# Performance work log

Measured on AMD Instinct MI355X. Metric: run time of the kernel, lower is better.

## Reference

```python
import jax, jax.numpy as jnp
import numpy as np


def setup_inputs() -> dict:
    key = jax.random.key(0)
    ks = jax.random.split(key, 20)
    B, P, ENC = 128, 196, 512
    DEC, ATT, EMB, V, S1 = 512, 256, 256, 5000, 257
    s = 0.02
    inp = {
        "features": jax.random.normal(ks[0], (B, P, ENC), jnp.float32),
        "captions": jax.random.randint(ks[1], (B, S1), 0, V),
        "emb": jax.random.normal(ks[2], (V, EMB), jnp.float32) * s,
        "Ua_w": jax.random.normal(ks[3], (ENC, ATT), jnp.float32) * s,
        "Ua_b": jnp.zeros((ATT,), jnp.float32),
        "Wa_w": jax.random.normal(ks[4], (DEC, ATT), jnp.float32) * s,
        "Wa_b": jnp.zeros((ATT,), jnp.float32),
        "va_w": jax.random.normal(ks[5], (ATT,), jnp.float32) * s,
        "va_b": jnp.zeros((), jnp.float32),
        "ih_w": jax.random.normal(ks[6], (ENC, DEC), jnp.float32) * s,
        "ih_b": jnp.zeros((DEC,), jnp.float32),
        "ic_w": jax.random.normal(ks[7], (ENC, DEC), jnp.float32) * s,
        "ic_b": jnp.zeros((DEC,), jnp.float32),
        "W_ih": jax.random.normal(ks[8], (EMB + ENC, 4 * DEC), jnp.float32) * s,
        "b_ih": jnp.zeros((4 * DEC,), jnp.float32),
        "W_hh": jax.random.normal(ks[9], (DEC, 4 * DEC), jnp.float32) * s,
        "b_hh": jnp.zeros((4 * DEC,), jnp.float32),
        "fcn_w": jax.random.normal(ks[10], (DEC, V), jnp.float32) * s,
        "fcn_b": jnp.zeros((V,), jnp.float32),
    }
    return inp


def reference(features, captions, emb, Ua_w, Ua_b, Wa_w, Wa_b, va_w, va_b,
              ih_w, ih_b, ic_w, ic_b, W_ih, b_ih, W_hh, b_hh, fcn_w, fcn_b):
    # embeds: [B, S+1, E]; we consume embeds[:, :S]
    embeds = emb[captions]
    mean_f = features.mean(axis=1)                      # [B, ENC]
    h0 = mean_f @ ih_w + ih_b                           # [B, DEC]
    c0 = mean_f @ ic_w + ic_b
    Uf = features @ Ua_w + Ua_b                         # [B, P, ATT] precomputed

    def step(carry, x_emb):
        h, c = carry
        att = jnp.tanh(Uf + (h @ Wa_w + Wa_b)[:, None, :])   # [B, P, ATT]
        scores = att @ va_w + va_b                            # [B, P]
        alpha = jax.nn.softmax(scores, axis=1)
        context = jnp.einsum('bp,bpe->be', alpha, features)   # [B, ENC]
        x = jnp.concatenate([x_emb, context], axis=1)         # [B, EMB+ENC]
        gates = x @ W_ih + b_ih + h @ W_hh + b_hh             # [B, 4*DEC]
        i, f, g, o = jnp.split(gates, 4, axis=1)
        c = jax.nn.sigmoid(f) * c + jax.nn.sigmoid(i) * jnp.tanh(g)
        h = jax.nn.sigmoid(o) * jnp.tanh(c)
        out = h @ fcn_w + fcn_b                               # dropout is identity (p=0)
        return (h, c), out

    xs = jnp.swapaxes(embeds[:, :-1], 0, 1)             # [S, B, EMB]
    _, preds = jax.lax.scan(step, (h0, c0), xs)         # [S, B, V]
    return jnp.swapaxes(preds, 0, 1)                    # [B, S, V]
```

## Files before the change

kernel.cpp:

```cpp
#include <hip/hip_runtime.h>
#include <hip/hip_bf16.h>

#define B 128
#define P 196
#define PP 200
#define ENC 512
#define DEC 512
#define ATT 256
#define EMB 256
#define V 5000
#define S 256
#define S1 257
#define NG 2048
#define KS 16

typedef __attribute__((ext_vector_type(4))) short s4v;
typedef __attribute__((ext_vector_type(8))) short s8v;

__device__ __forceinline__ float bf2f(short u) {
    unsigned int x = ((unsigned int)(unsigned short)u) << 16;
    float f; __builtin_memcpy(&f, &x, 4); return f;
}

__global__ __launch_bounds__(256) void k_mean(const float* __restrict__ feat,
                                              float* __restrict__ mean_f) {
    int idx = blockIdx.x * 256 + threadIdx.x;
    int b = idx >> 9, e = idx & 511;
    const float* fp = feat + (size_t)b * P * ENC + e;
    float s = 0.f;
    for (int p = 0; p < P; ++p) s += fp[(size_t)p * ENC];
    mean_f[idx] = s * (1.0f / (float)P);
}

__global__ __launch_bounds__(256) void k_init_hc(const float* __restrict__ mean_f,
        const float* __restrict__ ih_w, const float* __restrict__ ih_b,
        const float* __restrict__ ic_w, const float* __restrict__ ic_b,
        float* __restrict__ h, float* __restrict__ c) {
    int idx = blockIdx.x * 256 + threadIdx.x;
    int b = idx >> 9, d = idx & 511;
    const float* mf = mean_f + (size_t)b * ENC;
    float sh = ih_b[d], sc = ic_b[d];
    for (int e = 0; e < ENC; ++e) {
        float m = mf[e];
        sh = fmaf(m, ih_w[(size_t)e * DEC + d], sh);
        sc = fmaf(m, ic_w[(size_t)e * DEC + d], sc);
    }
    h[idx] = sh; c[idx] = sc;
}

__global__ __launch_bounds__(256) void k_uf(const float* __restrict__ feat,
        const float* __restrict__ Ua_w, const float* __restrict__ Ua_b,
        __hip_bfloat16* __restrict__ Uf) {
    int row0 = blockIdx.x * 8;
    int a = threadIdx.x;
    __shared__ float fs[8][ENC];
    for (int i = threadIdx.x; i < 8 * ENC; i += 256) {
        int r = i >> 9, e = i & 511;
        fs[r][e] = feat[(size_t)(row0 + r) * ENC + e];
    }
    __syncthreads();
    float acc[8];
    float bia = Ua_b[a];
#pragma unroll
    for (int r = 0; r < 8; ++r) acc[r] = bia;
    for (int e = 0; e < ENC; ++e) {
        float w = Ua_w[(size_t)e * ATT + a];
#pragma unroll
        for (int r = 0; r < 8; ++r) acc[r] = fmaf(fs[r][e], w, acc[r]);
    }
#pragma unroll
    for (int r = 0; r < 8; ++r)
        Uf[(size_t)(row0 + r) * ATT + a] = __float2bfloat16(acc[r]);
}

__global__ __launch_bounds__(512) void k_featT(const float* __restrict__ feat,
        __hip_bfloat16* __restrict__ featT) {
    int b = blockIdx.x, p0 = blockIdx.y * 8;
    int e = threadIdx.x;
    __hip_bfloat16 v[8];
#pragma unroll
    for (int i = 0; i < 8; ++i) {
        int p = p0 + i;
        float f = (p < P) ? feat[((size_t)b * P + p) * ENC + e] : 0.f;
        v[i] = __float2bfloat16(f);
    }
    __builtin_memcpy(&featT[((size_t)b * ENC + e) * PP + p0], v, 16);
}

__global__ __launch_bounds__(256) void k_wacvt(const float* __restrict__ w,
        __hip_bfloat16* __restrict__ wb) {
    int i = blockIdx.x * 256 + threadIdx.x;
    wb[i] = __float2bfloat16(w[i]);
}

__global__ __launch_bounds__(256) void k_gemb(const float* __restrict__ emb,
        const int* __restrict__ captions, const float* __restrict__ W_ih,
        __hip_bfloat16* __restrict__ Gemb) {
    __shared__ float As[16][128];
    __shared__ float Bs[16][128];
    __shared__ int rowcap[128];
    int m0 = blockIdx.x * 128;
    int n0 = blockIdx.y * 128;
    int tid = threadIdx.x;
    if (tid < 128) {
        int m = m0 + tid;
        rowcap[tid] = captions[(size_t)(m & 127) * S1 + (m >> 7)];
    }
    __syncthreads();
    int tx = tid & 15, ty = tid >> 4;
    float acc[8][8];
#pragma unroll
    for (int i = 0; i < 8; ++i)
#pragma unroll
        for (int j = 0; j < 8; ++j) acc[i][j] = 0.f;
    int arow = tid >> 1, ak = (tid & 1) * 8;
    int bkk = tid >> 4, bn = (tid & 15) * 8;
    for (int k0 = 0; k0 < EMB; k0 += 16) {
        {
            const float* ap = emb + (size_t)rowcap[arow] * EMB + k0 + ak;
            float4 v0 = *(const float4*)ap;
            float4 v1 = *(const float4*)(ap + 4);
            As[ak + 0][arow] = v0.x; As[ak + 1][arow] = v0.y;
            As[ak + 2][arow] = v0.z; As[ak + 3][arow] = v0.w;
            As[ak + 4][arow] = v1.x; As[ak + 5][arow] = v1.y;
            As[ak + 6][arow] = v1.z; As[ak + 7][arow] = v1.w;
        }
        {
            const float* bp = W_ih + (size_t)(k0 + bkk) * NG + n0 + bn;
            *(float4*)&Bs[bkk][bn] = *(const float4*)bp;
            *(float4*)&Bs[bkk][bn + 4] = *(const float4*)(bp + 4);
        }
        __syncthreads();
#pragma unroll
        for (int kk = 0; kk < 16; ++kk) {
            float4 a0 = *(const float4*)&As[kk][ty * 8];
            float4 a1 = *(const float4*)&As[kk][ty * 8 + 4];
            float4 b0 = *(const float4*)&Bs[kk][tx * 8];
            float4 b1 = *(const float4*)&Bs[kk][tx * 8 + 4];
            float av[8] = {a0.x, a0.y, a0.z, a0.w, a1.x, a1.y, a1.z, a1.w};
            float bv[8] = {b0.x, b0.y, b0.z, b0.w, b1.x, b1.y, b1.z, b1.w};
#pragma unroll
            for (int i = 0; i < 8; ++i)
#pragma unroll
                for (int j = 0; j < 8; ++j)
                    acc[i][j] = fmaf(av[i], bv[j], acc[i][j]);
        }
        __syncthreads();
    }
#pragma unroll
    for (int i = 0; i < 8; ++i) {
        __hip_bfloat16* gp = Gemb + (size_t)(m0 + ty * 8 + i) * NG + n0 + tx * 8;
#pragma unroll
        for (int j = 0; j < 8; ++j) gp[j] = __float2bfloat16(acc[i][j]);
    }
}

__global__ __launch_bounds__(1024) void k_attn_cell(
        const float* __restrict__ partials, const __hip_bfloat16* __restrict__ Gemb,
        const float* __restrict__ b_ih, const float* __restrict__ b_hh,
        float* __restrict__ h, const float* __restrict__ cr, float* __restrict__ cw,
        float* __restrict__ Hall,
        const __hip_bfloat16* __restrict__ Wa_wb, const float* __restrict__ Wa_b,
        const __hip_bfloat16* __restrict__ Uf, const __hip_bfloat16* __restrict__ featT,
        const float* __restrict__ va_w, const float* __restrict__ va_b,
        float* __restrict__ ctxp, float* __restrict__ mlp,
        int t, int use_gemb, int use_hall) {
    int g = blockIdx.x;
    int b = g >> 1, half = g & 1;
    int tid = threadIdx.x;
    int base = half ? 96 : 0;
    int cnt  = half ? 100 : 96;
    __shared__ float hs[DEC];
    __shared__ float wahp[4][ATT];
    __shared__ float wahs[ATT];
    __shared__ float sc[104];
    __shared__ float red[4];
    __shared__ float cpart[2][ENC];

    if (t > 0) {
        if (tid < DEC) {
            int d = tid;
            float s0 = b_ih[d]           + b_hh[d];
            float s1 = b_ih[d + DEC]     + b_hh[d + DEC];
            float s2 = b_ih[d + 2 * DEC] + b_hh[d + 2 * DEC];
            float s3 = b_ih[d + 3 * DEC] + b_hh[d + 3 * DEC];
#pragma unroll
            for (int ks = 0; ks < KS; ++ks) {
                const float* pp = partials + ((size_t)ks * B + b) * NG + d;
                s0 += pp[0]; s1 += pp[DEC]; s2 += pp[2 * DEC]; s3 += pp[3 * DEC];
            }
            if (use_gemb) {
                const __hip_bfloat16* gp = Gemb + ((size_t)(t - 1) * B + b) * NG + d;
                s0 += __bfloat162float(gp[0]);
                s1 += __bfloat162float(gp[DEC]);
                s2 += __bfloat162float(gp[2 * DEC]);
                s3 += __bfloat162float(gp[3 * DEC]);
            }
            size_t gidx = (size_t)b * DEC + d;
            float ii = 1.f / (1.f + __expf(-s0));
            float ff = 1.f / (1.f + __expf(-s1));
            float gg = tanhf(s2);
            float oo = 1.f / (1.f + __expf(-s3));
            float cn = ff * cr[gidx] + ii * gg;
            float hn = oo * tanhf(cn);
            hs[d] = hn;
            if (half == 0) {
                cw[gidx] = cn;
                h[gidx] = hn;
                if (use_hall) Hall[((size_t)(t - 1) * B + b) * DEC + d] = hn;
            }
        }
    } else {
        if (tid < DEC) hs[tid] = h[(size_t)b * DEC + tid];
    }
    __syncthreads();
    if (t == S) return;

    {
        int a = tid & 255, q = tid >> 8;
        float acc = 0.f;
        const __hip_bfloat16* wp = Wa_wb + (size_t)(q * 128) * ATT + a;
        const float* hq = &hs[q * 128];
#pragma unroll 4
        for (int dd = 0; dd < 128; ++dd)
            acc = fmaf(hq[dd], bf2f(*(const short*)&wp[(size_t)dd * ATT]), acc);
        wahp[q][a] = acc;
    }
    __syncthreads();
    if (tid < ATT)
        wahs[tid] = Wa_b[tid] + wahp[0][tid] + wahp[1][tid] + wahp[2][tid] + wahp[3][tid];
    __syncthreads();

    {
        int w = tid >> 6, lane = tid & 63;
        float4 wv = *(const float4*)&wahs[lane * 4];
        float4 vv = *(const float4*)&va_w[lane * 4];
        float vb = va_b[0];
        for (int pl = w; pl < cnt; pl += 16) {
            const __hip_bfloat16* ufp = Uf + ((size_t)b * P + base + pl) * ATT + lane * 4;
            s4v u4 = *(const s4v*)ufp;
            float ssc = vv.x * tanhf(bf2f(u4.x) + wv.x) + vv.y * tanhf(bf2f(u4.y) + wv.y)
                      + vv.z * tanhf(bf2f(u4.z) + wv.z) + vv.w * tanhf(bf2f(u4.w) + wv.w);
#pragma unroll
            for (int off = 32; off; off >>= 1) ssc += __shfl_down(ssc, off);
            if (lane == 0) sc[pl] = ssc + vb;
        }
    }
    __syncthreads();

    {
        int lane = tid & 63;
        float v = (tid < cnt) ? sc[tid] : -1e30f;
        if (tid < 128) {
            float m = v;
#pragma unroll
            for (int off = 32; off; off >>= 1) m = fmaxf(m, __shfl_down(m, off));
            if (lane == 0) red[tid >> 6] = m;
        }
        __syncthreads();
        float mh = fmaxf(red[0], red[1]);
        float e = (tid < cnt) ? __expf(v - mh) : 0.f;
        if (tid < 128) {
            float l = e;
#pragma unroll
            for (int off = 32; off; off >>= 1) l += __shfl_down(l, off);
            if (lane == 0) red[2 + (tid >> 6)] = l;
        }
        __syncthreads();
        if (tid < cnt) sc[tid] = e;
        else if (tid < 104) sc[tid] = 0.f;
        if (tid == 0) {
            mlp[((size_t)half * B + b) * 2 + 0] = mh;
            mlp[((size_t)half * B + b) * 2 + 1] = red[2] + red[3];
        }
    }
    __syncthreads();

    {
        int e = tid & 511, ph = tid >> 9;
        int start = half ? (ph ? 7 : 0) : (ph ? 6 : 0);
        int nch   = half ? (ph ? 6 : 7) : 6;
        float acc = 0.f;
        const __hip_bfloat16* fr = featT + ((size_t)b * ENC + e) * PP + base + start * 8;
        for (int ch = 0; ch < nch; ++ch) {
            s8v raw = *(const s8v*)(fr + ch * 8);
            const float* sp = &sc[(start + ch) * 8];
#pragma unroll
            for (int j = 0; j < 8; ++j)
                acc = fmaf(sp[j], bf2f(raw[j]), acc);
        }
        cpart[ph][e] = acc;
    }
    __syncthreads();
    if (tid < ENC)
        ctxp[((size_t)half * B + b) * ENC + tid] = cpart[0][tid] + cpart[1][tid];
}

__global__ __launch_bounds__(256) void k_gates(const float* __restrict__ emb,
        const int* __restrict__ captions, int t,
        const float* __restrict__ ctxp, const float* __restrict__ mlp,
        const float* __restrict__ h,
        const float* __restrict__ W_ih, const float* __restrict__ W_hh,
        float* __restrict__ partials, int use_gemb) {
    __shared__ float As[16][128];
    __shared__ float Bs[16][64];
    __shared__ float sw0[B], sw1[B];
    __shared__ int scap[B];
    int n0 = blockIdx.x * 64;
    int ks = blockIdx.y;
    int tid = threadIdx.x;
    int kch = use_gemb ? 64 : 80;
    if (tid < B) {
        float m0 = mlp[(size_t)tid * 2 + 0];
        float l0 = mlp[(size_t)tid * 2 + 1];
        float m1 = mlp[((size_t)B + tid) * 2 + 0];
        float l1 = mlp[((size_t)B + tid) * 2 + 1];
        float M = fmaxf(m0, m1);
        float e0 = __expf(m0 - M), e1 = __expf(m1 - M);
        float inv = 1.f / (l0 * e0 + l1 * e1);
        sw0[tid] = e0 * inv; sw1[tid] = e1 * inv;
        if (!use_gemb) scap[tid] = captions[(size_t)tid * S1 + t];
    }
    __syncthreads();
    int tx = tid & 15, ty = tid >> 4;
    float acc[8][4];
#pragma unroll
    for (int i = 0; i < 8; ++i)
#pragma unroll
        for (int j = 0; j < 4; ++j) acc[i][j] = 0.f;
    int arow = tid >> 1, ak = (tid & 1) * 8;
    int bkk = tid >> 4, bn = (tid & 15) * 4;
    for (int k0 = ks * kch; k0 < ks * kch + kch; k0 += 16) {
        {
            int k = k0 + ak;
            if (!use_gemb && k < EMB) {
                const float* ap = emb + (size_t)scap[arow] * EMB + k;
                float4 v0 = *(const float4*)ap;
                float4 v1 = *(const float4*)(ap + 4);
                As[ak + 0][arow] = v0.x; As[ak + 1][arow] = v0.y;
                As[ak + 2][arow] = v0.z; As[ak + 3][arow] = v0.w;
                As[ak + 4][arow] = v1.x; As[ak + 5][arow] = v1.y;
                As[ak + 6][arow] = v1.z; As[ak + 7][arow] = v1.w;
            } else {
                int kc = use_gemb ? k : (k - EMB);
                if (kc < ENC) {
                    const float* p0 = ctxp + (size_t)arow * ENC + kc;
                    const float* p1 = ctxp + ((size_t)B + arow) * ENC + kc;
                    float w0 = sw0[arow], w1 = sw1[arow];
                    float4 a0 = *(const float4*)p0;
                    float4 a1 = *(const float4*)(p0 + 4);
                    float4 b0 = *(const float4*)p1;
                    float4 b1 = *(const float4*)(p1 + 4);
                    As[ak + 0][arow] = a0.x * w0 + b0.x * w1;
                    As[ak + 1][arow] = a0.y * w0 + b0.y * w1;
                    As[ak + 2][arow] = a0.z * w0 + b0.z * w1;
                    As[ak + 3][arow] = a0.w * w0 + b0.w * w1;
                    As[ak + 4][arow] = a1.x * w0 + b1.x * w1;
                    As[ak + 5][arow] = a1.y * w0 + b1.y * w1;
                    As[ak + 6][arow] = a1.z * w0 + b1.z * w1;
                    As[ak + 7][arow] = a1.w * w0 + b1.w * w1;
                } else {
                    const float* ap = h + (size_t)arow * DEC + (kc - ENC);
                    float4 v0 = *(const float4*)ap;
                    float4 v1 = *(const float4*)(ap + 4);
                    As[ak + 0][arow] = v0.x; As[ak + 1][arow] = v0.y;
                    As[ak + 2][arow] = v0.z; As[ak + 3][arow] = v0.w;
                    As[ak + 4][arow] = v1.x; As[ak + 5][arow] = v1.y;
                    As[ak + 6][arow] = v1.z; As[ak + 7][arow] = v1.w;
                }
            }
        }
        {
            int k = k0 + bkk;
            const float* bp;
            if (use_gemb)
                bp = (k < ENC) ? W_ih + (size_t)(k + EMB) * NG + n0 + bn
                               : W_hh + (size_t)(k - ENC) * NG + n0 + bn;
            else
                bp = (k < EMB + ENC) ? W_ih + (size_t)k * NG + n0 + bn
                                     : W_hh + (size_t)(k - EMB - ENC) * NG + n0 + bn;
            *(float4*)&Bs[bkk][bn] = *(const float4*)bp;
        }
        __syncthreads();
#pragma unroll
        for (int kk = 0; kk < 16; ++kk) {
            float4 a0 = *(const float4*)&As[kk][ty * 8];
            float4 a1 = *(const float4*)&As[kk][ty * 8 + 4];
            float4 b0 = *(const float4*)&Bs[kk][tx * 4];
            float av[8] = {a0.x, a0.y, a0.z, a0.w, a1.x, a1.y, a1.z, a1.w};
            float bv[4] = {b0.x, b0.y, b0.z, b0.w};
#pragma unroll
            for (int i = 0; i < 8; ++i)
#pragma unroll
                for (int j = 0; j < 4; ++j)
                    acc[i][j] = fmaf(av[i], bv[j], acc[i][j]);
        }
        __syncthreads();
    }
#pragma unroll
    for (int i = 0; i < 8; ++i) {
        int mrow = ty * 8 + i;
        float* pp = partials + ((size_t)ks * B + mrow) * NG + n0 + tx * 4;
        *(float4*)pp = make_float4(acc[i][0], acc[i][1], acc[i][2], acc[i][3]);
    }
}

__global__ __launch_bounds__(256) void k_fcn(const float* __restrict__ A,
        const float* __restrict__ Bw, const float* __restrict__ bias,
        float* __restrict__ out, int t_fix) {
    __shared__ float As[16][128];
    __shared__ float Bs[16][128];
    int m0 = blockIdx.x * 128;
    int n0 = blockIdx.y * 128;
    int tid = threadIdx.x;
    int tx = tid & 15, ty = tid >> 4;
    float acc[8][8];
#pragma unroll
    for (int i = 0; i < 8; ++i)
#pragma unroll
        for (int j = 0; j < 8; ++j) acc[i][j] = 0.f;
    int arow = tid >> 1, ak = (tid & 1) * 8;
    int bkk = tid >> 4, bn = (tid & 15) * 8;
    const float4 z4 = make_float4(0.f, 0.f, 0.f, 0.f);
    for (int k0 = 0; k0 < DEC; k0 += 16) {
        {
            const float* ap = A + (size_t)(m0 + arow) * DEC + k0 + ak;
            float4 v0 = *(const float4*)ap;
            float4 v1 = *(const float4*)(ap + 4);
            As[ak + 0][arow] = v0.x; As[ak + 1][arow] = v0.y;
            As[ak + 2][arow] = v0.z; As[ak + 3][arow] = v0.w;
            As[ak + 4][arow] = v1.x; As[ak + 5][arow] = v1.y;
            As[ak + 6][arow] = v1.z; As[ak + 7][arow] = v1.w;
        }
        {
            int n4 = n0 + bn;
            const float* bp = Bw + (size_t)(k0 + bkk) * V + n4;
            float4 v0 = (n4 < V) ? *(const float4*)bp : z4;
            float4 v1 = (n4 + 4 < V) ? *(const float4*)(bp + 4) : z4;
            *(float4*)&Bs[bkk][bn] = v0;
            *(float4*)&Bs[bkk][bn + 4] = v1;
        }
        __syncthreads();
#pragma unroll
        for (int kk = 0; kk < 16; ++kk) {
            float4 a0 = *(const float4*)&As[kk][ty * 8];
            float4 a1 = *(const float4*)&As[kk][ty * 8 + 4];
            float4 b0 = *(const float4*)&Bs[kk][tx * 8];
            float4 b1 = *(const float4*)&Bs[kk][tx * 8 + 4];
            float av[8] = {a0.x, a0.y, a0.z, a0.w, a1.x, a1.y, a1.z, a1.w};
            float bv[8] = {b0.x, b0.y, b0.z, b0.w, b1.x, b1.y, b1.z, b1.w};
#pragma unroll
            for (int i = 0; i < 8; ++i)
#pragma unroll
                for (int j = 0; j < 8; ++j)
                    acc[i][j] = fmaf(av[i], bv[j], acc[i][j]);
        }
        __syncthreads();
    }
#pragma unroll
    for (int i = 0; i < 8; ++i) {
        int mrow = m0 + ty * 8 + i;
        int bb, tt;
        if (t_fix >= 0) { bb = mrow; tt = t_fix; }
        else            { tt = mrow >> 7; bb = mrow & 127; }
        float* op = out + ((size_t)bb * S + tt) * V + n0 + tx * 8;
#pragma unroll
        for (int j = 0; j < 8; ++j) {
            int n = n0 + tx * 8 + j;
            if (n < V) op[j] = acc[i][j] + bias[n];
        }
    }
}

extern "C" void kernel_launch(void* const* d_in, const int* in_sizes, int n_in,
                              void* d_out, int out_size, void* d_ws, size_t ws_size,
                              hipStream_t stream) {
    const float* features = (const float*)d_in[0];
    const int*   captions = (const int*)d_in[1];
    const float* emb      = (const float*)d_in[2];
    const float* Ua_w     = (const float*)d_in[3];
    const float* Ua_b     = (const float*)d_in[4];
    const float* Wa_w     = (const float*)d_in[5];
    const float* Wa_b     = (const float*)d_in[6];
    const float* va_w     = (const float*)d_in[7];
    const float* va_b     = (const float*)d_in[8];
    const float* ih_w     = (const float*)d_in[9];
    const float* ih_b     = (const float*)d_in[10];
    const float* ic_w     = (const float*)d_in[11];
    const float* ic_b     = (const float*)d_in[12];
    const float* W_ih     = (const float*)d_in[13];
    const float* b_ih     = (const float*)d_in[14];
    const float* W_hh     = (const float*)d_in[15];
    const float* b_hh     = (const float*)d_in[16];
    const float* fcn_w    = (const float*)d_in[17];
    const float* fcn_b    = (const float*)d_in[18];
    float* out = (float*)d_out;
    char* wsb  = (char*)d_ws;

    size_t off = 0;
    __hip_bfloat16* Uf    = (__hip_bfloat16*)(wsb + off); off += (size_t)B * P * ATT * 2;
    __hip_bfloat16* featT = (__hip_bfloat16*)(wsb + off); off += (size_t)B * ENC * PP * 2;
    __hip_bfloat16* Wa_wb = (__hip_bfloat16*)(wsb + off); off += (size_t)DEC * ATT * 2;
    float* partials = (float*)(wsb + off); off += (size_t)KS * B * NG * 4;
    float* hbuf     = (float*)(wsb + off); off += (size_t)B * DEC * 4;
    float* cbufA    = (float*)(wsb + off); off += (size_t)B * DEC * 4;
    float* cbufB    = (float*)(wsb + off); off += (size_t)B * DEC * 4;
    float* ctxp     = (float*)(wsb + off); off += (size_t)2 * B * ENC * 4;
    float* mlp      = (float*)(wsb + off); off += 4096;
    float* meanf    = ctxp;
    size_t need_min = off;
    float* Hall     = (float*)(wsb + off); off += (size_t)S * B * DEC * 4;
    size_t need_hall = off;
    __hip_bfloat16* Gemb = (__hip_bfloat16*)(wsb + off);
    off += (size_t)S * B * NG * 2;
    size_t need_gemb = off;

    (void)need_min;
    int use_hall = ws_size >= need_hall;
    int use_gemb = ws_size >= need_gemb;

    k_mean<<<256, 256, 0, stream>>>(features, meanf);
    k_init_hc<<<256, 256, 0, stream>>>(meanf, ih_w, ih_b, ic_w, ic_b, hbuf, cbufA);
    k_uf<<<3136, 256, 0, stream>>>(features, Ua_w, Ua_b, Uf);
    k_featT<<<dim3(128, 25), 512, 0, stream>>>(features, featT);
    k_wacvt<<<512, 256, 0, stream>>>(Wa_w, Wa_wb);
    if (use_gemb)
        k_gemb<<<dim3(256, 16), 256, 0, stream>>>(emb, captions, W_ih, Gemb);

    for (int t = 0; t <= S; ++t) {
        const float* crd = (t & 1) ? cbufA : cbufB;
        float*       cwr = (t & 1) ? cbufB : cbufA;
        k_attn_cell<<<256, 1024, 0, stream>>>(partials, Gemb, b_ih, b_hh,
                hbuf, crd, cwr, Hall, Wa_wb, Wa_b, Uf, featT, va_w, va_b,
                ctxp, mlp, t, use_gemb, use_hall);
        if (t < S)
            k_gates<<<dim3(32, KS), 256, 0, stream>>>(emb, captions, t, ctxp, mlp,
                    hbuf, W_ih, W_hh, partials, use_gemb);
        if (!use_hall && t > 0)
            k_fcn<<<dim3(1, 40), 256, 0, stream>>>(hbuf, fcn_w, fcn_b, out, t - 1);
    }
    if (use_hall)
        k_fcn<<<dim3(256, 40), 256, 0, stream>>>(Hall, fcn_w, fcn_b, out, -1);
}
```

Before: 14.77 ms.

## Double-buffer gates GEMM, prefetch Uf into LDS, use fast tanh

The gates GEMM kernel now keeps two shared-memory buffers and loads the next K-chunk into registers while computing on the current one, leaving one barrier per chunk instead of two. In the attention-cell kernel, threads 512-1023 copy the per-batch Uf slice into LDS while the first 512 threads finish the LSTM cell update, and the score loop then reads Uf from LDS. tanhf is replaced with a clamped exp/rcp approximation in the cell and attention paths. This adds LDS usage (about 51KB for ufs) and slightly changes numerics.

```diff
diff --git a/kernel.cpp b/kernel.cpp
--- a/kernel.cpp
+++ b/kernel.cpp
@@ -20,6 +20,12 @@
 __device__ __forceinline__ float bf2f(short u) {
     unsigned int x = ((unsigned int)(unsigned short)u) << 16;
     float f; __builtin_memcpy(&f, &x, 4); return f;
+}
+
+__device__ __forceinline__ float tanhf_fast(float x) {
+    float xx = fminf(fmaxf(x, -15.f), 15.f);
+    float t = __expf(2.f * xx);
+    return (t - 1.f) * __builtin_amdgcn_rcpf(t + 1.f);
 }
 
 __global__ __launch_bounds__(256) void k_mean(const float* __restrict__ feat,
@@ -170,6 +176,7 @@
     int tid = threadIdx.x;
     int base = half ? 96 : 0;
     int cnt  = half ? 100 : 96;
+    __shared__ short ufs[100][ATT];
     __shared__ float hs[DEC];
     __shared__ float wahp[4][ATT];
     __shared__ float wahs[ATT];
@@ -177,8 +184,8 @@
     __shared__ float red[4];
     __shared__ float cpart[2][ENC];
 
-    if (t > 0) {
-        if (tid < DEC) {
+    if (tid < 512) {
+        if (t > 0) {
             int d = tid;
             float s0 = b_ih[d]           + b_hh[d];
             float s1 = b_ih[d + DEC]     + b_hh[d + DEC];
@@ -199,19 +206,25 @@
             size_t gidx = (size_t)b * DEC + d;
             float ii = 1.f / (1.f + __expf(-s0));
             float ff = 1.f / (1.f + __expf(-s1));
-            float gg = tanhf(s2);
+            float gg = tanhf_fast(s2);
             float oo = 1.f / (1.f + __expf(-s3));
             float cn = ff * cr[gidx] + ii * gg;
-            float hn = oo * tanhf(cn);
+            float hn = oo * tanhf_fast(cn);
             hs[d] = hn;
             if (half == 0) {
                 cw[gidx] = cn;
                 h[gidx] = hn;
                 if (use_hall) Hall[((size_t)(t - 1) * B + b) * DEC + d] = hn;
             }
-        }
-    } else {
-        if (tid < DEC) hs[tid] = h[(size_t)b * DEC + tid];
+        } else {
+            hs[tid] = h[(size_t)b * DEC + tid];
+        }
+    } else if (t < S) {
+        const __hip_bfloat16* ub = Uf + ((size_t)b * P + base) * ATT;
+        for (int i = tid - 512; i < cnt * 32; i += 512) {
+            int p = i >> 5, c = (i & 31) * 8;
+            *(s8v*)&ufs[p][c] = *(const s8v*)(ub + (size_t)p * ATT + c);
+        }
     }
     __syncthreads();
     if (t == S) return;
@@ -237,10 +250,11 @@
         float4 vv = *(const float4*)&va_w[lane * 4];
         float vb = va_b[0];
         for (int pl = w; pl < cnt; pl += 16) {
-            const __hip_bfloat16* ufp = Uf + ((size_t)b * P + base + pl) * ATT + lane * 4;
-            s4v u4 = *(const s4v*)ufp;
-            float ssc = vv.x * tanhf(bf2f(u4.x) + wv.x) + vv.y * tanhf(bf2f(u4.y) + wv.y)
-                      + vv.z * tanhf(bf2f(u4.z) + wv.z) + vv.w * tanhf(bf2f(u4.w) + wv.w);
+            s4v u4 = *(const s4v*)&ufs[pl][lane * 4];
+            float ssc = vv.x * tanhf_fast(bf2f(u4.x) + wv.x)
+                      + vv.y * tanhf_fast(bf2f(u4.y) + wv.y)
+                      + vv.z * tanhf_fast(bf2f(u4.z) + wv.z)
+                      + vv.w * tanhf_fast(bf2f(u4.w) + wv.w);
 #pragma unroll
             for (int off = 32; off; off >>= 1) ssc += __shfl_down(ssc, off);
             if (lane == 0) sc[pl] = ssc + vb;
@@ -302,8 +316,8 @@
         const float* __restrict__ h,
         const float* __restrict__ W_ih, const float* __restrict__ W_hh,
         float* __restrict__ partials, int use_gemb) {
-    __shared__ float As[16][128];
-    __shared__ float Bs[16][64];
+    __shared__ float As[2][16][128];
+    __shared__ float Bs[2][16][64];
     __shared__ float sw0[B], sw1[B];
     __shared__ int scap[B];
     int n0 = blockIdx.x * 64;
@@ -321,7 +335,6 @@
         sw0[tid] = e0 * inv; sw1[tid] = e1 * inv;
         if (!use_gemb) scap[tid] = captions[(size_t)tid * S1 + t];
     }
-    __syncthreads();
     int tx = tid & 15, ty = tid >> 4;
     float acc[8][4];
 #pragma unroll
@@ -330,17 +343,69 @@
         for (int j = 0; j < 4; ++j) acc[i][j] = 0.f;
     int arow = tid >> 1, ak = (tid & 1) * 8;
     int bkk = tid >> 4, bn = (tid & 15) * 4;
-    for (int k0 = ks * kch; k0 < ks * kch + kch; k0 += 16) {
-        {
+    int kbase = ks * kch;
+    int nch = kch >> 4;
+    float rA[8];
+    float4 rB;
+    __syncthreads();
+
+    {
+        int k = kbase + ak;
+        if (!use_gemb && k < EMB) {
+            const float* ap = emb + (size_t)scap[arow] * EMB + k;
+            float4 v0 = *(const float4*)ap;
+            float4 v1 = *(const float4*)(ap + 4);
+            rA[0] = v0.x; rA[1] = v0.y; rA[2] = v0.z; rA[3] = v0.w;
+            rA[4] = v1.x; rA[5] = v1.y; rA[6] = v1.z; rA[7] = v1.w;
+        } else {
+            int kc = use_gemb ? k : (k - EMB);
+            if (kc < ENC) {
+                const float* p0 = ctxp + (size_t)arow * ENC + kc;
+                const float* p1 = ctxp + ((size_t)B + arow) * ENC + kc;
+                float w0 = sw0[arow], w1 = sw1[arow];
+                float4 a0 = *(const float4*)p0;
+                float4 a1 = *(const float4*)(p0 + 4);
+                float4 b0 = *(const float4*)p1;
+                float4 b1 = *(const float4*)(p1 + 4);
+                rA[0] = a0.x * w0 + b0.x * w1; rA[1] = a0.y * w0 + b0.y * w1;
+                rA[2] = a0.z * w0 + b0.z * w1; rA[3] = a0.w * w0 + b0.w * w1;
+                rA[4] = a1.x * w0 + b1.x * w1; rA[5] = a1.y * w0 + b1.y * w1;
+                rA[6] = a1.z * w0 + b1.z * w1; rA[7] = a1.w * w0 + b1.w * w1;
+            } else {
+                const float* ap = h + (size_t)arow * DEC + (kc - ENC);
+                float4 v0 = *(const float4*)ap;
+                float4 v1 = *(const float4*)(ap + 4);
+                rA[0] = v0.x; rA[1] = v0.y; rA[2] = v0.z; rA[3] = v0.w;
+                rA[4] = v1.x; rA[5] = v1.y; rA[6] = v1.z; rA[7] = v1.w;
+            }
+        }
+        int kb = kbase + bkk;
+        const float* bp;
+        if (use_gemb)
+            bp = (kb < ENC) ? W_ih + (size_t)(kb + EMB) * NG + n0 + bn
+                            : W_hh + (size_t)(kb - ENC) * NG + n0 + bn;
+        else
+            bp = (kb < EMB + ENC) ? W_ih + (size_t)kb * NG + n0 + bn
+                                  : W_hh + (size_t)(kb - EMB - ENC) * NG + n0 + bn;
+        rB = *(const float4*)bp;
+    }
+#pragma unroll
+    for (int i = 0; i < 8; ++i) As[0][ak + i][arow] = rA[i];
+    *(float4*)&Bs[0][bkk][bn] = rB;
+    __syncthreads();
+
+    for (int c = 0; c < nch; ++c) {
+        int cur = c & 1;
+        bool more = (c + 1 < nch);
+        if (more) {
+            int k0 = kbase + (c + 1) * 16;
             int k = k0 + ak;
             if (!use_gemb && k < EMB) {
                 const float* ap = emb + (size_t)scap[arow] * EMB + k;
                 float4 v0 = *(const float4*)ap;
                 float4 v1 = *(const float4*)(ap + 4);
-                As[ak + 0][arow] = v0.x; As[ak + 1][arow] = v0.y;
-                As[ak + 2][arow] = v0.z; As[ak + 3][arow] = v0.w;
-                As[ak + 4][arow] = v1.x; As[ak + 5][arow] = v1.y;
-                As[ak + 6][arow] = v1.z; As[ak + 7][arow] = v1.w;
+                rA[0] = v0.x; rA[1] = v0.y; rA[2] = v0.z; rA[3] = v0.w;
+                rA[4] = v1.x; rA[5] = v1.y; rA[6] = v1.z; rA[7] = v1.w;
             } else {
                 int kc = use_gemb ? k : (k - EMB);
                 if (kc < ENC) {
@@ -351,42 +416,33 @@
                     float4 a1 = *(const float4*)(p0 + 4);
                     float4 b0 = *(const float4*)p1;
                     float4 b1 = *(const float4*)(p1 + 4);
-                    As[ak + 0][arow] = a0.x * w0 + b0.x * w1;
-                    As[ak + 1][arow] = a0.y * w0 + b0.y * w1;
-                    As[ak + 2][arow] = a0.z * w0 + b0.z * w1;
-                    As[ak + 3][arow] = a0.w * w0 + b0.w * w1;
-                    As[ak + 4][arow] = a1.x * w0 + b1.x * w1;
-                    As[ak + 5][arow] = a1.y * w0 + b1.y * w1;
-                    As[ak + 6][arow] = a1.z * w0 + b1.z * w1;
-                    As[ak + 7][arow] = a1.w * w0 + b1.w * w1;
+                    rA[0] = a0.x * w0 + b0.x * w1; rA[1] = a0.y * w0 + b0.y * w1;
+                    rA[2] = a0.z * w0 + b0.z * w1; rA[3] = a0.w * w0 + b0.w * w1;
+                    rA[4] = a1.x * w0 + b1.x * w1; rA[5] = a1.y * w0 + b1.y * w1;
+                    rA[6] = a1.z * w0 + b1.z * w1; rA[7] = a1.w * w0 + b1.w * w1;
                 } else {
                     const float* ap = h + (size_t)arow * DEC + (kc - ENC);
                     float4 v0 = *(const float4*)ap;
                     float4 v1 = *(const float4*)(ap + 4);
-                    As[ak + 0][arow] = v0.x; As[ak + 1][arow] = v0.y;
-                    As[ak + 2][arow] = v0.z; As[ak + 3][arow] = v0.w;
-                    As[ak + 4][arow] = v1.x; As[ak + 5][arow] = v1.y;
-                    As[ak + 6][arow] = v1.z; As[ak + 7][arow] = v1.w;
+                    rA[0] = v0.x; rA[1] = v0.y; rA[2] = v0.z; rA[3] = v0.w;
+                    rA[4] = v1.x; rA[5] = v1.y; rA[6] = v1.z; rA[7] = v1.w;
                 }
             }
-        }
-        {
-            int k = k0 + bkk;
+            int kb = k0 + bkk;
             const float* bp;
             if (use_gemb)
-                bp = (k < ENC) ? W_ih + (size_t)(k + EMB) * NG + n0 + bn
-                               : W_hh + (size_t)(k - ENC) * NG + n0 + bn;
+                bp = (kb < ENC) ? W_ih + (size_t)(kb + EMB) * NG + n0 + bn
+                                : W_hh + (size_t)(kb - ENC) * NG + n0 + bn;
             else
-                bp = (k < EMB + ENC) ? W_ih + (size_t)k * NG + n0 + bn
-                                     : W_hh + (size_t)(k - EMB - ENC) * NG + n0 + bn;
-            *(float4*)&Bs[bkk][bn] = *(const float4*)bp;
-        }
-        __syncthreads();
+                bp = (kb < EMB + ENC) ? W_ih + (size_t)kb * NG + n0 + bn
+                                      : W_hh + (size_t)(kb - EMB - ENC) * NG + n0 + bn;
+            rB = *(const float4*)bp;
+        }
 #pragma unroll
         for (int kk = 0; kk < 16; ++kk) {
-            float4 a0 = *(const float4*)&As[kk][ty * 8];
-            float4 a1 = *(const float4*)&As[kk][ty * 8 + 4];
-            float4 b0 = *(const float4*)&Bs[kk][tx * 4];
+            float4 a0 = *(const float4*)&As[cur][kk][ty * 8];
+            float4 a1 = *(const float4*)&As[cur][kk][ty * 8 + 4];
+            float4 b0 = *(const float4*)&Bs[cur][kk][tx * 4];
             float av[8] = {a0.x, a0.y, a0.z, a0.w, a1.x, a1.y, a1.z, a1.w};
             float bv[4] = {b0.x, b0.y, b0.z, b0.w};
 #pragma unroll
@@ -395,7 +451,12 @@
                 for (int j = 0; j < 4; ++j)
                     acc[i][j] = fmaf(av[i], bv[j], acc[i][j]);
         }
-        __syncthreads();
+        if (more) {
+#pragma unroll
+            for (int i = 0; i < 8; ++i) As[cur ^ 1][ak + i][arow] = rA[i];
+            *(float4*)&Bs[cur ^ 1][bkk][bn] = rB;
+            __syncthreads();
+        }
     }
 #pragma unroll
     for (int i = 0; i < 8; ++i) {
```

Result: faster. 14.11 ms (-4.5%).
